# Kernel optimization log

Hardware: AMD Instinct MI355X
Metric: run time of the kernel (lower is better)

## Reference

```python
import jax, jax.numpy as jnp
import numpy as np
import math

H = 16          # num_attention_heads
DH = 64         # attention_head_size
HID = 1024      # hidden_size


def _rotate_half(x):
    # stack([-x[...,1::2], x[...,::2]], -1).reshape_as(x)
    return jnp.stack([-x[..., 1::2], x[..., ::2]], axis=-1).reshape(x.shape)


def _apply_rope(sinusoidal_pos, q, k):
    sin, cos = jnp.split(sinusoidal_pos, 2, axis=-1)            # [1,1,S,DH/2] each
    sin_pos = jnp.stack([sin, sin], axis=-1).reshape(sinusoidal_pos.shape)
    cos_pos = jnp.stack([cos, cos], axis=-1).reshape(sinusoidal_pos.shape)
    q = q * cos_pos + _rotate_half(q) * sin_pos
    k = k * cos_pos + _rotate_half(k) * sin_pos
    return q, k


def _split_heads(x):
    B, S, _ = x.shape
    return x.reshape(B, S, H, DH).transpose(0, 2, 1, 3)         # [B,H,S,DH]


def setup_inputs() -> dict:
    key = jax.random.key(0)
    ks = jax.random.split(key, 5)
    B, S = 4, 2048
    x = jax.random.normal(ks[0], (B, S, HID), dtype=jnp.float32)
    attention_mask = jnp.zeros((B, 1, 1, S), dtype=jnp.float32)
    sinusoidal_pos = jax.random.normal(ks[1], (1, 1, S, DH), dtype=jnp.float32)
    scale = 1.0 / math.sqrt(HID)
    Wq = jax.random.normal(ks[2], (HID, HID), dtype=jnp.float32) * scale
    Wk = jax.random.normal(ks[3], (HID, HID), dtype=jnp.float32) * scale
    Wv = jax.random.normal(ks[4], (HID, HID), dtype=jnp.float32) * scale
    bq = jnp.zeros((HID,), dtype=jnp.float32)
    bk = jnp.zeros((HID,), dtype=jnp.float32)
    bv = jnp.zeros((HID,), dtype=jnp.float32)
    return {"x": x, "attention_mask": attention_mask, "sinusoidal_pos": sinusoidal_pos,
            "Wq": Wq, "bq": bq, "Wk": Wk, "bk": bk, "Wv": Wv, "bv": bv}


def reference(x, attention_mask, sinusoidal_pos, Wq, bq, Wk, bk, Wv, bv):
    # QKV projections (torch Linear: x @ W.T + b)
    q = _split_heads(x @ Wq.T + bq)                             # [B,H,S,DH]
    k = _split_heads(x @ Wk.T + bk)
    v = _split_heads(x @ Wv.T + bv)
    q, k = _apply_rope(sinusoidal_pos, q, k)
    scores = jnp.einsum('bhsd,bhtd->bhst', q, k) / math.sqrt(DH) + attention_mask
    probs = jax.nn.softmax(scores, axis=-1)                     # dropout p=0.0 -> identity
    ctx = jnp.einsum('bhst,bhtd->bhsd', probs, v)               # [B,H,S,DH]
    B, _, S, _ = ctx.shape
    return ctx.transpose(0, 2, 1, 3).reshape(B, S, HID)
```

## Files before the change

kernel.cpp:

```cpp
#include <hip/hip_runtime.h>
#include <stdint.h>

#define BATCH 4
#define SEQ   2048
#define NHEAD 16
#define DHEAD 64
#define HID   1024

typedef __bf16 bf16x8 __attribute__((ext_vector_type(8)));
typedef __bf16 bf16x4 __attribute__((ext_vector_type(4)));
typedef float  f32x4  __attribute__((ext_vector_type(4)));

__device__ __forceinline__ bf16x8 load8f(const float* p) {
  const f32x4 a = ((const f32x4*)p)[0];
  const f32x4 b = ((const f32x4*)p)[1];
  bf16x8 r;
#pragma unroll
  for (int i = 0; i < 4; ++i) r[i] = (__bf16)a[i];
#pragma unroll
  for (int i = 0; i < 4; ++i) r[4 + i] = (__bf16)b[i];
  return r;
}

__device__ __forceinline__ void gload_lds16(const __bf16* g, __bf16* l) {
  __builtin_amdgcn_global_load_lds(
      (const __attribute__((address_space(1))) uint32_t*)g,
      (__attribute__((address_space(3))) uint32_t*)l,
      16, 0, 0);
}

#define XUNITS 1048576
#define WUNITS 131072

__global__ __launch_bounds__(256) void cvt_fused_kernel(
    const float* __restrict__ x,
    const float* __restrict__ Wq, const float* __restrict__ Wk,
    const float* __restrict__ Wv,
    __bf16* __restrict__ xb, __bf16* __restrict__ Wb) {
  const int i = blockIdx.x * 256 + threadIdx.x;
  const float* s;
  __bf16* d;
  if (i < XUNITS) {
    s = x + (size_t)i * 8;
    d = xb + (size_t)i * 8;
  } else {
    const int j = i - XUNITS;
    const int w = j >> 17;
    const int o = j & (WUNITS - 1);
    s = (w == 0 ? Wq : w == 1 ? Wk : Wv) + (size_t)o * 8;
    d = Wb + ((size_t)w << 20) + (size_t)o * 8;
  }
  *(bf16x8*)d = load8f(s);
}

#define ASTRIDE 40
#define BK 32

__global__ __launch_bounds__(512) void qkv_bf16_kernel(
    const __bf16* __restrict__ xb, const __bf16* __restrict__ Wb,
    const float* __restrict__ bq, const float* __restrict__ bk,
    const float* __restrict__ bv, const float* __restrict__ sp,
    float* __restrict__ qout, __bf16* __restrict__ Kws, __bf16* __restrict__ Vws)
{
  const int widx = blockIdx.z;
  const __bf16* __restrict__ W    = Wb + (size_t)widx * HID * HID;
  const float*  __restrict__ bias = (widx == 0) ? bq : (widx == 1) ? bk : bv;

  const int m0   = blockIdx.y * 128;
  const int n0   = blockIdx.x * 128;
  const int tid  = threadIdx.x;
  const int lane = tid & 63;
  const int quad = lane >> 4;
  const int l16  = lane & 15;
  const int wave = tid >> 6;
  const int wr   = wave >> 1, wc = wave & 1;

  __shared__ __align__(16) __bf16 As[2][128 * BK];
  __shared__ __align__(16) __bf16 Bs[2][128 * BK];

  const int srow = wave * 16 + (lane >> 2);
  const int scol = (lane & 3) * 8;
  const __bf16* aglb = xb + (size_t)(m0 + srow) * HID + scol;
  const __bf16* bglb = W  + (size_t)(n0 + srow) * HID + scol;
  const int woff = wave * 512;

  f32x4 acc[2][4];
  const f32x4 z = {0.f, 0.f, 0.f, 0.f};
#pragma unroll
  for (int i = 0; i < 2; ++i)
#pragma unroll
    for (int j = 0; j < 4; ++j) acc[i][j] = z;

  gload_lds16(aglb, &As[0][woff]);
  gload_lds16(bglb, &Bs[0][woff]);
  __syncthreads();

#pragma unroll 1
  for (int k0 = 0; k0 < HID; k0 += 2 * BK) {
    {
      gload_lds16(aglb + (k0 + BK), &As[1][woff]);
      gload_lds16(bglb + (k0 + BK), &Bs[1][woff]);

      bf16x8 af[2], bfr[4];
#pragma unroll
      for (int mt = 0; mt < 2; ++mt)
        af[mt] = *(const bf16x8*)(&As[0][(wr * 32 + mt * 16 + l16) * BK + quad * 8]);
#pragma unroll
      for (int nt = 0; nt < 4; ++nt)
        bfr[nt] = *(const bf16x8*)(&Bs[0][(wc * 64 + nt * 16 + l16) * BK + quad * 8]);

      if (widx < 2) {
#pragma unroll
        for (int mt = 0; mt < 2; ++mt)
#pragma unroll
          for (int nt = 0; nt < 4; ++nt)
            acc[mt][nt] = __builtin_amdgcn_mfma_f32_16x16x32_bf16(af[mt], bfr[nt], acc[mt][nt], 0, 0, 0);
      } else {
#pragma unroll
        for (int mt = 0; mt < 2; ++mt)
#pragma unroll
          for (int nt = 0; nt < 4; ++nt)
            acc[mt][nt] = __builtin_amdgcn_mfma_f32_16x16x32_bf16(bfr[nt], af[mt], acc[mt][nt], 0, 0, 0);
      }
      __syncthreads();
    }
    {
      if (k0 + 2 * BK < HID) {
        gload_lds16(aglb + (k0 + 2 * BK), &As[0][woff]);
        gload_lds16(bglb + (k0 + 2 * BK), &Bs[0][woff]);
      }

      bf16x8 af[2], bfr[4];
#pragma unroll
      for (int mt = 0; mt < 2; ++mt)
        af[mt] = *(const bf16x8*)(&As[1][(wr * 32 + mt * 16 + l16) * BK + quad * 8]);
#pragma unroll
      for (int nt = 0; nt < 4; ++nt)
        bfr[nt] = *(const bf16x8*)(&Bs[1][(wc * 64 + nt * 16 + l16) * BK + quad * 8]);

      if (widx < 2) {
#pragma unroll
        for (int mt = 0; mt < 2; ++mt)
#pragma unroll
          for (int nt = 0; nt < 4; ++nt)
            acc[mt][nt] = __builtin_amdgcn_mfma_f32_16x16x32_bf16(af[mt], bfr[nt], acc[mt][nt], 0, 0, 0);
      } else {
#pragma unroll
        for (int mt = 0; mt < 2; ++mt)
#pragma unroll
          for (int nt = 0; nt < 4; ++nt)
            acc[mt][nt] = __builtin_amdgcn_mfma_f32_16x16x32_bf16(bfr[nt], af[mt], acc[mt][nt], 0, 0, 0);
      }
      __syncthreads();
    }
  }

  if (widx < 2) {
#pragma unroll
    for (int mt = 0; mt < 2; ++mt) {
#pragma unroll
      for (int nt = 0; nt < 4; ++nt) {
        const int n = n0 + wc * 64 + nt * 16 + l16;
        const int h = n >> 6, d = n & 63;
        const float bval = bias[n];
#pragma unroll
        for (int v = 0; v < 4; ++v) {
          const int m = m0 + wr * 32 + mt * 16 + quad * 4 + v;
          const int b = m >> 11, s = m & (SEQ - 1);
          float val = acc[mt][nt][v] + bval;
          float p  = __shfl_xor(val, 1);
          float sn = sp[s * 64 + (d >> 1)];
          float cs = sp[s * 64 + 32 + (d >> 1)];
          val = val * cs + ((d & 1) ? p : -p) * sn;
          if (widx == 0) {
            qout[((size_t)b * SEQ + s) * HID + n] = val;
          } else {
            Kws[(((size_t)b * NHEAD + h) * SEQ + s) * DHEAD + d] = (__bf16)val;
          }
        }
      }
    }
  } else {
#pragma unroll
    for (int mt = 0; mt < 2; ++mt) {
#pragma unroll
      for (int nt = 0; nt < 4; ++nt) {
        const int m = m0 + wr * 32 + mt * 16 + l16;
        const int b = m >> 11, s = m & (SEQ - 1);
#pragma unroll
        for (int v = 0; v < 4; ++v) {
          const int n = n0 + wc * 64 + nt * 16 + quad * 4 + v;
          const int h = n >> 6, d = n & 63;
          float val = acc[mt][nt][v] + bias[n];
          Vws[(((size_t)b * NHEAD + h) * DHEAD + d) * SEQ + s] = (__bf16)val;
        }
      }
    }
  }
}

__global__ __launch_bounds__(512) void qkv_f32_kernel(
    const float* __restrict__ x,
    const float* __restrict__ Wq, const float* __restrict__ bq,
    const float* __restrict__ Wk, const float* __restrict__ bk,
    const float* __restrict__ Wv, const float* __restrict__ bv,
    const float* __restrict__ sp,
    float* __restrict__ qout, __bf16* __restrict__ Kws, __bf16* __restrict__ Vws)
{
  const int widx = blockIdx.z;
  const float* __restrict__ W    = (widx == 0) ? Wq : (widx == 1) ? Wk : Wv;
  const float* __restrict__ bias = (widx == 0) ? bq : (widx == 1) ? bk : bv;

  const int m0   = blockIdx.y * 128;
  const int n0   = blockIdx.x * 128;
  const int tid  = threadIdx.x;
  const int lane = tid & 63;
  const int quad = lane >> 4;
  const int l16  = lane & 15;
  const int wave = tid >> 6;
  const int wr   = wave >> 1, wc = wave & 1;

  __shared__ __align__(16) __bf16 As[128 * ASTRIDE];
  __shared__ __align__(16) __bf16 Bs[128 * ASTRIDE];

  const int srow = tid >> 2;
  const int scb  = tid & 3;

  f32x4 acc[2][4];
  const f32x4 z = {0.f, 0.f, 0.f, 0.f};
#pragma unroll
  for (int i = 0; i < 2; ++i)
#pragma unroll
    for (int j = 0; j < 4; ++j) acc[i][j] = z;

  bf16x8 areg = load8f(x + (size_t)(m0 + srow) * HID + scb * 8);
  bf16x8 breg = load8f(W + (size_t)(n0 + srow) * HID + scb * 8);

  for (int k0 = 0; k0 < HID; k0 += 32) {
    __syncthreads();
    *(bf16x8*)(As + srow * ASTRIDE + scb * 8) = areg;
    *(bf16x8*)(Bs + srow * ASTRIDE + scb * 8) = breg;
    __syncthreads();

    if (k0 + 32 < HID) {
      areg = load8f(x + (size_t)(m0 + srow) * HID + (k0 + 32) + scb * 8);
      breg = load8f(W + (size_t)(n0 + srow) * HID + (k0 + 32) + scb * 8);
    }

    bf16x8 af[2], bfr[4];
#pragma unroll
    for (int mt = 0; mt < 2; ++mt)
      af[mt] = *(const bf16x8*)(As + (wr * 32 + mt * 16 + l16) * ASTRIDE + quad * 8);
#pragma unroll
    for (int nt = 0; nt < 4; ++nt)
      bfr[nt] = *(const bf16x8*)(Bs + (wc * 64 + nt * 16 + l16) * ASTRIDE + quad * 8);

    if (widx < 2) {
#pragma unroll
      for (int mt = 0; mt < 2; ++mt)
#pragma unroll
        for (int nt = 0; nt < 4; ++nt)
          acc[mt][nt] = __builtin_amdgcn_mfma_f32_16x16x32_bf16(af[mt], bfr[nt], acc[mt][nt], 0, 0, 0);
    } else {
#pragma unroll
      for (int mt = 0; mt < 2; ++mt)
#pragma unroll
        for (int nt = 0; nt < 4; ++nt)
          acc[mt][nt] = __builtin_amdgcn_mfma_f32_16x16x32_bf16(bfr[nt], af[mt], acc[mt][nt], 0, 0, 0);
    }
  }

  if (widx < 2) {
#pragma unroll
    for (int mt = 0; mt < 2; ++mt) {
#pragma unroll
      for (int nt = 0; nt < 4; ++nt) {
        const int n = n0 + wc * 64 + nt * 16 + l16;
        const int h = n >> 6, d = n & 63;
        const float bval = bias[n];
#pragma unroll
        for (int v = 0; v < 4; ++v) {
          const int m = m0 + wr * 32 + mt * 16 + quad * 4 + v;
          const int b = m >> 11, s = m & (SEQ - 1);
          float val = acc[mt][nt][v] + bval;
          float p  = __shfl_xor(val, 1);
          float sn = sp[s * 64 + (d >> 1)];
          float cs = sp[s * 64 + 32 + (d >> 1)];
          val = val * cs + ((d & 1) ? p : -p) * sn;
          if (widx == 0) {
            qout[((size_t)b * SEQ + s) * HID + n] = val;
          } else {
            Kws[(((size_t)b * NHEAD + h) * SEQ + s) * DHEAD + d] = (__bf16)val;
          }
        }
      }
    }
  } else {
#pragma unroll
    for (int mt = 0; mt < 2; ++mt) {
#pragma unroll
      for (int nt = 0; nt < 4; ++nt) {
        const int m = m0 + wr * 32 + mt * 16 + l16;
        const int b = m >> 11, s = m & (SEQ - 1);
#pragma unroll
        for (int v = 0; v < 4; ++v) {
          const int n = n0 + wc * 64 + nt * 16 + quad * 4 + v;
          const int h = n >> 6, d = n & 63;
          float val = acc[mt][nt][v] + bias[n];
          Vws[(((size_t)b * NHEAD + h) * DHEAD + d) * SEQ + s] = (__bf16)val;
        }
      }
    }
  }
}

#define KT 64
#define QSTR 72
#define LOG2E 1.44269504088896340736f
#define PSHIFT 12.0f

__global__ __launch_bounds__(512) void attn_kernel(
    float* __restrict__ qo,
    const __bf16* __restrict__ Kws, const __bf16* __restrict__ Vws,
    const float* __restrict__ mask)
{
  const int q0   = blockIdx.x * 128;
  const int bh   = blockIdx.y;
  const int b    = bh >> 4, h = bh & 15;
  const int tid  = threadIdx.x;
  const int lane = tid & 63;
  const int wave = tid >> 6;
  const int quad = lane >> 4;
  const int l16  = lane & 15;

  __shared__ __align__(16) __bf16 Ks[2][64 * QSTR];
  __shared__ __align__(16) __bf16 Vts[2][64 * QSTR];
  __shared__ __align__(16) __bf16 PS[128 * QSTR];

  const __bf16* kbase = Kws + (size_t)bh * SEQ * DHEAD;
  const __bf16* vbase = Vws + (size_t)bh * DHEAD * SEQ;

  bf16x8 qf[2];
#pragma unroll
  for (int ks = 0; ks < 2; ++ks)
    qf[ks] = load8f(qo + ((size_t)b * SEQ + q0 + wave * 16 + l16) * HID
                       + h * DHEAD + ks * 32 + quad * 8);

  f32x4 o_acc[4];
  const f32x4 z = {0.f, 0.f, 0.f, 0.f};
#pragma unroll
  for (int i = 0; i < 4; ++i) o_acc[i] = z;
  float l_part = 0.f;

  const int qrow = tid >> 3;
  const int qcb  = tid & 7;
  const int soff = qrow * QSTR + qcb * 8;

  bf16x8 kreg = *(const bf16x8*)(kbase + (size_t)qrow * DHEAD + qcb * 8);
  bf16x8 vreg = *(const bf16x8*)(vbase + (size_t)qrow * SEQ + qcb * 8);
  *(bf16x8*)(&Ks[0][soff])  = kreg;
  *(bf16x8*)(&Vts[0][soff]) = vreg;
  kreg = *(const bf16x8*)(kbase + (size_t)(KT + qrow) * DHEAD + qcb * 8);
  vreg = *(const bf16x8*)(vbase + (size_t)qrow * SEQ + KT + qcb * 8);
  __syncthreads();

  const float SC2 = 0.125f * LOG2E;
  int cur = 0;

  for (int t0 = 0; t0 < SEQ; t0 += KT) {
    const __bf16* kcur = &Ks[cur][0];
    const __bf16* vcur = &Vts[cur][0];

    if (t0 + KT < SEQ) {
      *(bf16x8*)(&Ks[cur ^ 1][soff])  = kreg;
      *(bf16x8*)(&Vts[cur ^ 1][soff]) = vreg;
    }
    if (t0 + 2 * KT < SEQ) {
      kreg = *(const bf16x8*)(kbase + (size_t)(t0 + 2 * KT + qrow) * DHEAD + qcb * 8);
      vreg = *(const bf16x8*)(vbase + (size_t)qrow * SEQ + (t0 + 2 * KT) + qcb * 8);
    }

    f32x4 sc[4];
#pragma unroll
    for (int nt = 0; nt < 4; ++nt) sc[nt] = z;

    __builtin_amdgcn_s_setprio(1);
#pragma unroll
    for (int ks = 0; ks < 2; ++ks) {
      bf16x8 kf[4];
#pragma unroll
      for (int nt = 0; nt < 4; ++nt)
        kf[nt] = *(const bf16x8*)(kcur + (nt * 16 + l16) * QSTR + ks * 32 + quad * 8);
#pragma unroll
      for (int nt = 0; nt < 4; ++nt)
        sc[nt] = __builtin_amdgcn_mfma_f32_16x16x32_bf16(kf[nt], qf[ks], sc[nt], 0, 0, 0);
    }
    __builtin_amdgcn_s_setprio(0);

    f32x4 mv4[4];
#pragma unroll
    for (int nt = 0; nt < 4; ++nt)
      mv4[nt] = *(const f32x4*)(mask + b * SEQ + t0 + nt * 16 + quad * 4);

    const int prow = wave * 16 + l16;
#pragma unroll
    for (int nt = 0; nt < 4; ++nt) {
      bf16x4 pk;
#pragma unroll
      for (int v = 0; v < 4; ++v) {
        const float p = __builtin_amdgcn_exp2f(sc[nt][v] * SC2 + mv4[nt][v] * LOG2E - PSHIFT);
        l_part += p;
        pk[v] = (__bf16)p;
      }
      *(bf16x4*)(PS + prow * QSTR + nt * 16 + quad * 4) = pk;
    }

    __builtin_amdgcn_s_setprio(1);
#pragma unroll
    for (int ks2 = 0; ks2 < 2; ++ks2) {
      bf16x8 pf = *(const bf16x8*)(PS + prow * QSTR + ks2 * 32 + quad * 8);
      bf16x8 vf[4];
#pragma unroll
      for (int db = 0; db < 4; ++db)
        vf[db] = *(const bf16x8*)(vcur + (db * 16 + l16) * QSTR + ks2 * 32 + quad * 8);
#pragma unroll
      for (int db = 0; db < 4; ++db)
        o_acc[db] = __builtin_amdgcn_mfma_f32_16x16x32_bf16(vf[db], pf, o_acc[db], 0, 0, 0);
    }
    __builtin_amdgcn_s_setprio(0);

    __syncthreads();
    cur ^= 1;
  }

  l_part += __shfl_xor(l_part, 16);
  l_part += __shfl_xor(l_part, 32);
  const float inv = 1.0f / l_part;

  const int s = q0 + wave * 16 + l16;
  float* op = qo + ((size_t)b * SEQ + s) * HID + h * DHEAD + quad * 4;
#pragma unroll
  for (int db = 0; db < 4; ++db) {
    f32x4 val = o_acc[db];
    val[0] *= inv; val[1] *= inv; val[2] *= inv; val[3] *= inv;
    *(f32x4*)(op + db * 16) = val;
  }
}

extern "C" void kernel_launch(void* const* d_in, const int* in_sizes, int n_in,
                              void* d_out, int out_size, void* d_ws, size_t ws_size,
                              hipStream_t stream) {
  const float* x    = (const float*)d_in[0];
  const float* mask = (const float*)d_in[1];
  const float* sp   = (const float*)d_in[2];
  const float* Wq   = (const float*)d_in[3];
  const float* bq   = (const float*)d_in[4];
  const float* Wk   = (const float*)d_in[5];
  const float* bk   = (const float*)d_in[6];
  const float* Wv   = (const float*)d_in[7];
  const float* bv   = (const float*)d_in[8];
  float* out = (float*)d_out;

  const size_t per = (size_t)BATCH * NHEAD * SEQ * DHEAD;
  const size_t wel = (size_t)3 * HID * HID;
  __bf16* Kws = (__bf16*)d_ws;
  __bf16* Vws = Kws + per;

  const size_t need = (2 * per + per + wel) * sizeof(__bf16);
  if (ws_size >= need) {
    __bf16* xb = Vws + per;
    __bf16* Wb = xb + per;
    cvt_fused_kernel<<<5632, 256, 0, stream>>>(x, Wq, Wk, Wv, xb, Wb);
    qkv_bf16_kernel<<<dim3(8, 64, 3), 512, 0, stream>>>(
        xb, Wb, bq, bk, bv, sp, out, Kws, Vws);
  } else {
    qkv_f32_kernel<<<dim3(8, 64, 3), 512, 0, stream>>>(
        x, Wq, bq, Wk, bk, Wv, bv, sp, out, Kws, Vws);
  }
  attn_kernel<<<dim3(16, 64), 512, 0, stream>>>(out, Kws, Vws, mask);
}
```

Baseline: 308.0 us.

## Load K/V fragments directly from global into registers, drop LDS staging

The attention kernel stops staging K and V tiles through double-buffered shared memory and instead has each wave load its MFMA fragments straight from global memory into registers. One register array is reused for K and then V, and the next K tile is loaded at the end of each iteration. The block shrinks to 256 threads covering 64 queries, and the grid doubles, so the per-tile __syncthreads goes away and LDS use drops. In exchange, each wave now reads K/V itself, with no sharing across waves in a block, so global/L2 traffic rises. Load latency is only partly hidden by issuing loads ahead of their use.

After: 662.8 us. 2.15x slower.

```diff
diff --git a/kernel.cpp b/kernel.cpp
--- a/kernel.cpp
+++ b/kernel.cpp
@@ -319,12 +319,12 @@
 #define LOG2E 1.44269504088896340736f
 #define PSHIFT 12.0f
 
-__global__ __launch_bounds__(512) void attn_kernel(
+__global__ __launch_bounds__(256) void attn_kernel(
     float* __restrict__ qo,
     const __bf16* __restrict__ Kws, const __bf16* __restrict__ Vws,
     const float* __restrict__ mask)
 {
-  const int q0   = blockIdx.x * 128;
+  const int q0   = blockIdx.x * 64;
   const int bh   = blockIdx.y;
   const int b    = bh >> 4, h = bh & 15;
   const int tid  = threadIdx.x;
@@ -333,9 +333,7 @@
   const int quad = lane >> 4;
   const int l16  = lane & 15;
 
-  __shared__ __align__(16) __bf16 Ks[2][64 * QSTR];
-  __shared__ __align__(16) __bf16 Vts[2][64 * QSTR];
-  __shared__ __align__(16) __bf16 PS[128 * QSTR];
+  __shared__ __align__(16) __bf16 PS[64 * QSTR];
 
   const __bf16* kbase = Kws + (size_t)bh * SEQ * DHEAD;
   const __bf16* vbase = Vws + (size_t)bh * DHEAD * SEQ;
@@ -352,57 +350,45 @@
   for (int i = 0; i < 4; ++i) o_acc[i] = z;
   float l_part = 0.f;
 
-  const int qrow = tid >> 3;
-  const int qcb  = tid & 7;
-  const int soff = qrow * QSTR + qcb * 8;
-
-  bf16x8 kreg = *(const bf16x8*)(kbase + (size_t)qrow * DHEAD + qcb * 8);
-  bf16x8 vreg = *(const bf16x8*)(vbase + (size_t)qrow * SEQ + qcb * 8);
-  *(bf16x8*)(&Ks[0][soff])  = kreg;
-  *(bf16x8*)(&Vts[0][soff]) = vreg;
-  kreg = *(const bf16x8*)(kbase + (size_t)(KT + qrow) * DHEAD + qcb * 8);
-  vreg = *(const bf16x8*)(vbase + (size_t)qrow * SEQ + KT + qcb * 8);
-  __syncthreads();
+  const __bf16* kfb = kbase + (size_t)l16 * DHEAD + quad * 8;
+  const __bf16* vfb = vbase + (size_t)l16 * SEQ + quad * 8;
+
+  bf16x8 kv[2][4];
+
+#pragma unroll
+  for (int ks = 0; ks < 2; ++ks)
+#pragma unroll
+    for (int nt = 0; nt < 4; ++nt)
+      kv[ks][nt] = *(const bf16x8*)(kfb + (size_t)(nt * 16) * DHEAD + ks * 32);
 
   const float SC2 = 0.125f * LOG2E;
-  int cur = 0;
-
+  const int prow = wave * 16 + l16;
+
+#pragma unroll 1
   for (int t0 = 0; t0 < SEQ; t0 += KT) {
-    const __bf16* kcur = &Ks[cur][0];
-    const __bf16* vcur = &Vts[cur][0];
-
-    if (t0 + KT < SEQ) {
-      *(bf16x8*)(&Ks[cur ^ 1][soff])  = kreg;
-      *(bf16x8*)(&Vts[cur ^ 1][soff]) = vreg;
-    }
-    if (t0 + 2 * KT < SEQ) {
-      kreg = *(const bf16x8*)(kbase + (size_t)(t0 + 2 * KT + qrow) * DHEAD + qcb * 8);
-      vreg = *(const bf16x8*)(vbase + (size_t)qrow * SEQ + (t0 + 2 * KT) + qcb * 8);
-    }
-
     f32x4 sc[4];
 #pragma unroll
     for (int nt = 0; nt < 4; ++nt) sc[nt] = z;
 
     __builtin_amdgcn_s_setprio(1);
 #pragma unroll
-    for (int ks = 0; ks < 2; ++ks) {
-      bf16x8 kf[4];
+    for (int ks = 0; ks < 2; ++ks)
 #pragma unroll
       for (int nt = 0; nt < 4; ++nt)
-        kf[nt] = *(const bf16x8*)(kcur + (nt * 16 + l16) * QSTR + ks * 32 + quad * 8);
-#pragma unroll
-      for (int nt = 0; nt < 4; ++nt)
-        sc[nt] = __builtin_amdgcn_mfma_f32_16x16x32_bf16(kf[nt], qf[ks], sc[nt], 0, 0, 0);
-    }
+        sc[nt] = __builtin_amdgcn_mfma_f32_16x16x32_bf16(kv[ks][nt], qf[ks], sc[nt], 0, 0, 0);
     __builtin_amdgcn_s_setprio(0);
+
+#pragma unroll
+    for (int ks2 = 0; ks2 < 2; ++ks2)
+#pragma unroll
+      for (int db = 0; db < 4; ++db)
+        kv[ks2][db] = *(const bf16x8*)(vfb + (size_t)(db * 16) * SEQ + t0 + ks2 * 32);
 
     f32x4 mv4[4];
 #pragma unroll
     for (int nt = 0; nt < 4; ++nt)
       mv4[nt] = *(const f32x4*)(mask + b * SEQ + t0 + nt * 16 + quad * 4);
 
-    const int prow = wave * 16 + l16;
 #pragma unroll
     for (int nt = 0; nt < 4; ++nt) {
       bf16x4 pk;
@@ -419,18 +405,19 @@
 #pragma unroll
     for (int ks2 = 0; ks2 < 2; ++ks2) {
       bf16x8 pf = *(const bf16x8*)(PS + prow * QSTR + ks2 * 32 + quad * 8);
-      bf16x8 vf[4];
 #pragma unroll
       for (int db = 0; db < 4; ++db)
-        vf[db] = *(const bf16x8*)(vcur + (db * 16 + l16) * QSTR + ks2 * 32 + quad * 8);
-#pragma unroll
-      for (int db = 0; db < 4; ++db)
-        o_acc[db] = __builtin_amdgcn_mfma_f32_16x16x32_bf16(vf[db], pf, o_acc[db], 0, 0, 0);
+        o_acc[db] = __builtin_amdgcn_mfma_f32_16x16x32_bf16(kv[ks2][db], pf, o_acc[db], 0, 0, 0);
     }
     __builtin_amdgcn_s_setprio(0);
 
-    __syncthreads();
-    cur ^= 1;
+    if (t0 + KT < SEQ) {
+#pragma unroll
+      for (int ks = 0; ks < 2; ++ks)
+#pragma unroll
+        for (int nt = 0; nt < 4; ++nt)
+          kv[ks][nt] = *(const bf16x8*)(kfb + (size_t)(t0 + KT + nt * 16) * DHEAD + ks * 32);
+    }
   }
 
   l_part += __shfl_xor(l_part, 16);
@@ -477,5 +464,5 @@
     qkv_f32_kernel<<<dim3(8, 64, 3), 512, 0, stream>>>(
         x, Wq, bq, Wk, bk, Wv, bv, sp, out, Kws, Vws);
   }
-  attn_kernel<<<dim3(16, 64), 512, 0, stream>>>(out, Kws, Vws, mask);
-}
+  attn_kernel<<<dim3(32, 64), 256, 0, stream>>>(out, Kws, Vws, mask);
+}
```

## Enlarge QKV GEMM M-tile to 256 and single-buffer attention K/V tiles

Applied to the files above, without the earlier changes.

The bf16 QKV projection kernel now computes a 256x128 output tile per block, with each wave holding 4x4 MFMA accumulators, and the grid is halved in M. This raises arithmetic intensity per LDS load and reuses each loaded W tile across twice as many rows, at the cost of more registers (launch bounds hint of 4). Separately, the attention kernel drops double-buffered K/V LDS tiles for a single buffer with a register prefetch, cutting LDS use but adding a barrier between the store and the compute.

Result: slower. 742.5 us (+141.1%).

```diff
diff --git a/kernel.cpp b/kernel.cpp
--- a/kernel.cpp
+++ b/kernel.cpp
@@ -56,7 +56,7 @@
 #define ASTRIDE 40
 #define BK 32
 
-__global__ __launch_bounds__(512) void qkv_bf16_kernel(
+__global__ __launch_bounds__(512, 4) void qkv_bf16_kernel(
     const __bf16* __restrict__ xb, const __bf16* __restrict__ Wb,
     const float* __restrict__ bq, const float* __restrict__ bk,
     const float* __restrict__ bv, const float* __restrict__ sp,
@@ -66,6 +66,159 @@
   const __bf16* __restrict__ W    = Wb + (size_t)widx * HID * HID;
   const float*  __restrict__ bias = (widx == 0) ? bq : (widx == 1) ? bk : bv;
 
+  const int m0   = blockIdx.y * 256;
+  const int n0   = blockIdx.x * 128;
+  const int tid  = threadIdx.x;
+  const int lane = tid & 63;
+  const int quad = lane >> 4;
+  const int l16  = lane & 15;
+  const int wave = tid >> 6;
+  const int wr   = wave >> 1, wc = wave & 1;
+
+  __shared__ __align__(16) __bf16 As[2][256 * BK];
+  __shared__ __align__(16) __bf16 Bs[2][128 * BK];
+
+  const int arow0 = wave * 32 + (lane >> 2);
+  const int arow1 = wave * 32 + 16 + (lane >> 2);
+  const int brow  = wave * 16 + (lane >> 2);
+  const int scol  = (lane & 3) * 8;
+  const __bf16* aglb0 = xb + (size_t)(m0 + arow0) * HID + scol;
+  const __bf16* aglb1 = xb + (size_t)(m0 + arow1) * HID + scol;
+  const __bf16* bglb  = W  + (size_t)(n0 + brow) * HID + scol;
+  const int aoff0 = wave * 1024;
+  const int aoff1 = wave * 1024 + 512;
+  const int boff  = wave * 512;
+
+  f32x4 acc[4][4];
+  const f32x4 z = {0.f, 0.f, 0.f, 0.f};
+#pragma unroll
+  for (int i = 0; i < 4; ++i)
+#pragma unroll
+    for (int j = 0; j < 4; ++j) acc[i][j] = z;
+
+  gload_lds16(aglb0, &As[0][aoff0]);
+  gload_lds16(aglb1, &As[0][aoff1]);
+  gload_lds16(bglb,  &Bs[0][boff]);
+  __syncthreads();
+
+#pragma unroll 1
+  for (int k0 = 0; k0 < HID; k0 += 2 * BK) {
+    {
+      gload_lds16(aglb0 + (k0 + BK), &As[1][aoff0]);
+      gload_lds16(aglb1 + (k0 + BK), &As[1][aoff1]);
+      gload_lds16(bglb  + (k0 + BK), &Bs[1][boff]);
+
+      bf16x8 af[4], bfr[4];
+#pragma unroll
+      for (int mt = 0; mt < 4; ++mt)
+        af[mt] = *(const bf16x8*)(&As[0][(wr * 64 + mt * 16 + l16) * BK + quad * 8]);
+#pragma unroll
+      for (int nt = 0; nt < 4; ++nt)
+        bfr[nt] = *(const bf16x8*)(&Bs[0][(wc * 64 + nt * 16 + l16) * BK + quad * 8]);
+
+      if (widx < 2) {
+#pragma unroll
+        for (int mt = 0; mt < 4; ++mt)
+#pragma unroll
+          for (int nt = 0; nt < 4; ++nt)
+            acc[mt][nt] = __builtin_amdgcn_mfma_f32_16x16x32_bf16(af[mt], bfr[nt], acc[mt][nt], 0, 0, 0);
+      } else {
+#pragma unroll
+        for (int mt = 0; mt < 4; ++mt)
+#pragma unroll
+          for (int nt = 0; nt < 4; ++nt)
+            acc[mt][nt] = __builtin_amdgcn_mfma_f32_16x16x32_bf16(bfr[nt], af[mt], acc[mt][nt], 0, 0, 0);
+      }
+      __syncthreads();
+    }
+    {
+      if (k0 + 2 * BK < HID) {
+        gload_lds16(aglb0 + (k0 + 2 * BK), &As[0][aoff0]);
+        gload_lds16(aglb1 + (k0 + 2 * BK), &As[0][aoff1]);
+        gload_lds16(bglb  + (k0 + 2 * BK), &Bs[0][boff]);
+      }
+
+      bf16x8 af[4], bfr[4];
+#pragma unroll
+      for (int mt = 0; mt < 4; ++mt)
+        af[mt] = *(const bf16x8*)(&As[1][(wr * 64 + mt * 16 + l16) * BK + quad * 8]);
+#pragma unroll
+      for (int nt = 0; nt < 4; ++nt)
+        bfr[nt] = *(const bf16x8*)(&Bs[1][(wc * 64 + nt * 16 + l16) * BK + quad * 8]);
+
+      if (widx < 2) {
+#pragma unroll
+        for (int mt = 0; mt < 4; ++mt)
+#pragma unroll
+          for (int nt = 0; nt < 4; ++nt)
+            acc[mt][nt] = __builtin_amdgcn_mfma_f32_16x16x32_bf16(af[mt], bfr[nt], acc[mt][nt], 0, 0, 0);
+      } else {
+#pragma unroll
+        for (int mt = 0; mt < 4; ++mt)
+#pragma unroll
+          for (int nt = 0; nt < 4; ++nt)
+            acc[mt][nt] = __builtin_amdgcn_mfma_f32_16x16x32_bf16(bfr[nt], af[mt], acc[mt][nt], 0, 0, 0);
+      }
+      __syncthreads();
+    }
+  }
+
+  if (widx < 2) {
+#pragma unroll
+    for (int mt = 0; mt < 4; ++mt) {
+#pragma unroll
+      for (int nt = 0; nt < 4; ++nt) {
+        const int n = n0 + wc * 64 + nt * 16 + l16;
+        const int h = n >> 6, d = n & 63;
+        const float bval = bias[n];
+#pragma unroll
+        for (int v = 0; v < 4; ++v) {
+          const int m = m0 + wr * 64 + mt * 16 + quad * 4 + v;
+          const int b = m >> 11, s = m & (SEQ - 1);
+          float val = acc[mt][nt][v] + bval;
+          float p  = __shfl_xor(val, 1);
+          float sn = sp[s * 64 + (d >> 1)];
+          float cs = sp[s * 64 + 32 + (d >> 1)];
+          val = val * cs + ((d & 1) ? p : -p) * sn;
+          if (widx == 0) {
+            qout[((size_t)b * SEQ + s) * HID + n] = val;
+          } else {
+            Kws[(((size_t)b * NHEAD + h) * SEQ + s) * DHEAD + d] = (__bf16)val;
+          }
+        }
+      }
+    }
+  } else {
+#pragma unroll
+    for (int mt = 0; mt < 4; ++mt) {
+#pragma unroll
+      for (int nt = 0; nt < 4; ++nt) {
+        const int m = m0 + wr * 64 + mt * 16 + l16;
+        const int b = m >> 11, s = m & (SEQ - 1);
+#pragma unroll
+        for (int v = 0; v < 4; ++v) {
+          const int n = n0 + wc * 64 + nt * 16 + quad * 4 + v;
+          const int h = n >> 6, d = n & 63;
+          float val = acc[mt][nt][v] + bias[n];
+          Vws[(((size_t)b * NHEAD + h) * DHEAD + d) * SEQ + s] = (__bf16)val;
+        }
+      }
+    }
+  }
+}
+
+__global__ __launch_bounds__(512) void qkv_f32_kernel(
+    const float* __restrict__ x,
+    const float* __restrict__ Wq, const float* __restrict__ bq,
+    const float* __restrict__ Wk, const float* __restrict__ bk,
+    const float* __restrict__ Wv, const float* __restrict__ bv,
+    const float* __restrict__ sp,
+    float* __restrict__ qout, __bf16* __restrict__ Kws, __bf16* __restrict__ Vws)
+{
+  const int widx = blockIdx.z;
+  const float* __restrict__ W    = (widx == 0) ? Wq : (widx == 1) ? Wk : Wv;
+  const float* __restrict__ bias = (widx == 0) ? bq : (widx == 1) ? bk : bv;
+
   const int m0   = blockIdx.y * 128;
   const int n0   = blockIdx.x * 128;
   const int tid  = threadIdx.x;
@@ -75,14 +228,11 @@
   const int wave = tid >> 6;
   const int wr   = wave >> 1, wc = wave & 1;
 
-  __shared__ __align__(16) __bf16 As[2][128 * BK];
-  __shared__ __align__(16) __bf16 Bs[2][128 * BK];
-
-  const int srow = wave * 16 + (lane >> 2);
-  const int scol = (lane & 3) * 8;
-  const __bf16* aglb = xb + (size_t)(m0 + srow) * HID + scol;
-  const __bf16* bglb = W  + (size_t)(n0 + srow) * HID + scol;
-  const int woff = wave * 512;
+  __shared__ __align__(16) __bf16 As[128 * ASTRIDE];
+  __shared__ __align__(16) __bf16 Bs[128 * ASTRIDE];
+
+  const int srow = tid >> 2;
+  const int scb  = tid & 3;
 
   f32x4 acc[2][4];
   const f32x4 z = {0.f, 0.f, 0.f, 0.f};
@@ -91,67 +241,40 @@
 #pragma unroll
     for (int j = 0; j < 4; ++j) acc[i][j] = z;
 
-  gload_lds16(aglb, &As[0][woff]);
-  gload_lds16(bglb, &Bs[0][woff]);
-  __syncthreads();
-
-#pragma unroll 1
-  for (int k0 = 0; k0 < HID; k0 += 2 * BK) {
-    {
-      gload_lds16(aglb + (k0 + BK), &As[1][woff]);
-      gload_lds16(bglb + (k0 + BK), &Bs[1][woff]);
-
-      bf16x8 af[2], bfr[4];
+  bf16x8 areg = load8f(x + (size_t)(m0 + srow) * HID + scb * 8);
+  bf16x8 breg = load8f(W + (size_t)(n0 + srow) * HID + scb * 8);
+
+  for (int k0 = 0; k0 < HID; k0 += 32) {
+    __syncthreads();
+    *(bf16x8*)(As + srow * ASTRIDE + scb * 8) = areg;
+    *(bf16x8*)(Bs + srow * ASTRIDE + scb * 8) = breg;
+    __syncthreads();
+
+    if (k0 + 32 < HID) {
+      areg = load8f(x + (size_t)(m0 + srow) * HID + (k0 + 32) + scb * 8);
+      breg = load8f(W + (size_t)(n0 + srow) * HID + (k0 + 32) + scb * 8);
+    }
+
+    bf16x8 af[2], bfr[4];
+#pragma unroll
+    for (int mt = 0; mt < 2; ++mt)
+      af[mt] = *(const bf16x8*)(As + (wr * 32 + mt * 16 + l16) * ASTRIDE + quad * 8);
+#pragma unroll
+    for (int nt = 0; nt < 4; ++nt)
+      bfr[nt] = *(const bf16x8*)(Bs + (wc * 64 + nt * 16 + l16) * ASTRIDE + quad * 8);
+
+    if (widx < 2) {
 #pragma unroll
       for (int mt = 0; mt < 2; ++mt)
-        af[mt] = *(const bf16x8*)(&As[0][(wr * 32 + mt * 16 + l16) * BK + quad * 8]);
-#pragma unroll
-      for (int nt = 0; nt < 4; ++nt)
-        bfr[nt] = *(const bf16x8*)(&Bs[0][(wc * 64 + nt * 16 + l16) * BK + quad * 8]);
-
-      if (widx < 2) {
-#pragma unroll
-        for (int mt = 0; mt < 2; ++mt)
-#pragma unroll
-          for (int nt = 0; nt < 4; ++nt)
-            acc[mt][nt] = __builtin_amdgcn_mfma_f32_16x16x32_bf16(af[mt], bfr[nt], acc[mt][nt], 0, 0, 0);
-      } else {
-#pragma unroll
-        for (int mt = 0; mt < 2; ++mt)
-#pragma unroll
-          for (int nt = 0; nt < 4; ++nt)
-            acc[mt][nt] = __builtin_amdgcn_mfma_f32_16x16x32_bf16(bfr[nt], af[mt], acc[mt][nt], 0, 0, 0);
-      }
-      __syncthreads();
-    }
-    {
-      if (k0 + 2 * BK < HID) {
-        gload_lds16(aglb + (k0 + 2 * BK), &As[0][woff]);
-        gload_lds16(bglb + (k0 + 2 * BK), &Bs[0][woff]);
-      }
-
-      bf16x8 af[2], bfr[4];
+#pragma unroll
+        for (int nt = 0; nt < 4; ++nt)
+          acc[mt][nt] = __builtin_amdgcn_mfma_f32_16x16x32_bf16(af[mt], bfr[nt], acc[mt][nt], 0, 0, 0);
+    } else {
 #pragma unroll
       for (int mt = 0; mt < 2; ++mt)
-        af[mt] = *(const bf16x8*)(&As[1][(wr * 32 + mt * 16 + l16) * BK + quad * 8]);
-#pragma unroll
-      for (int nt = 0; nt < 4; ++nt)
-        bfr[nt] = *(const bf16x8*)(&Bs[1][(wc * 64 + nt * 16 + l16) * BK + quad * 8]);
-
-      if (widx < 2) {
-#pragma unroll
-        for (int mt = 0; mt < 2; ++mt)
-#pragma unroll
-          for (int nt = 0; nt < 4; ++nt)
-            acc[mt][nt] = __builtin_amdgcn_mfma_f32_16x16x32_bf16(af[mt], bfr[nt], acc[mt][nt], 0, 0, 0);
-      } else {
-#pragma unroll
-        for (int mt = 0; mt < 2; ++mt)
-#pragma unroll
-          for (int nt = 0; nt < 4; ++nt)
-            acc[mt][nt] = __builtin_amdgcn_mfma_f32_16x16x32_bf16(bfr[nt], af[mt], acc[mt][nt], 0, 0, 0);
-      }
-      __syncthreads();
+#pragma unroll
+        for (int nt = 0; nt < 4; ++nt)
+          acc[mt][nt] = __builtin_amdgcn_mfma_f32_16x16x32_bf16(bfr[nt], af[mt], acc[mt][nt], 0, 0, 0);
     }
   }
 
@@ -199,121 +322,6 @@
   }
 }
 
-__global__ __launch_bounds__(512) void qkv_f32_kernel(
-    const float* __restrict__ x,
-    const float* __restrict__ Wq, const float* __restrict__ bq,
-    const float* __restrict__ Wk, const float* __restrict__ bk,
-    const float* __restrict__ Wv, const float* __restrict__ bv,
-    const float* __restrict__ sp,
-    float* __restrict__ qout, __bf16* __restrict__ Kws, __bf16* __restrict__ Vws)
-{
-  const int widx = blockIdx.z;
-  const float* __restrict__ W    = (widx == 0) ? Wq : (widx == 1) ? Wk : Wv;
-  const float* __restrict__ bias = (widx == 0) ? bq : (widx == 1) ? bk : bv;
-
-  const int m0   = blockIdx.y * 128;
-  const int n0   = blockIdx.x * 128;
-  const int tid  = threadIdx.x;
-  const int lane = tid & 63;
-  const int quad = lane >> 4;
-  const int l16  = lane & 15;
-  const int wave = tid >> 6;
-  const int wr   = wave >> 1, wc = wave & 1;
-
-  __shared__ __align__(16) __bf16 As[128 * ASTRIDE];
-  __shared__ __align__(16) __bf16 Bs[128 * ASTRIDE];
-
-  const int srow = tid >> 2;
-  const int scb  = tid & 3;
-
-  f32x4 acc[2][4];
-  const f32x4 z = {0.f, 0.f, 0.f, 0.f};
-#pragma unroll
-  for (int i = 0; i < 2; ++i)
-#pragma unroll
-    for (int j = 0; j < 4; ++j) acc[i][j] = z;
-
-  bf16x8 areg = load8f(x + (size_t)(m0 + srow) * HID + scb * 8);
-  bf16x8 breg = load8f(W + (size_t)(n0 + srow) * HID + scb * 8);
-
-  for (int k0 = 0; k0 < HID; k0 += 32) {
-    __syncthreads();
-    *(bf16x8*)(As + srow * ASTRIDE + scb * 8) = areg;
-    *(bf16x8*)(Bs + srow * ASTRIDE + scb * 8) = breg;
-    __syncthreads();
-
-    if (k0 + 32 < HID) {
-      areg = load8f(x + (size_t)(m0 + srow) * HID + (k0 + 32) + scb * 8);
-      breg = load8f(W + (size_t)(n0 + srow) * HID + (k0 + 32) + scb * 8);
-    }
-
-    bf16x8 af[2], bfr[4];
-#pragma unroll
-    for (int mt = 0; mt < 2; ++mt)
-      af[mt] = *(const bf16x8*)(As + (wr * 32 + mt * 16 + l16) * ASTRIDE + quad * 8);
-#pragma unroll
-    for (int nt = 0; nt < 4; ++nt)
-      bfr[nt] = *(const bf16x8*)(Bs + (wc * 64 + nt * 16 + l16) * ASTRIDE + quad * 8);
-
-    if (widx < 2) {
-#pragma unroll
-      for (int mt = 0; mt < 2; ++mt)
-#pragma unroll
-        for (int nt = 0; nt < 4; ++nt)
-          acc[mt][nt] = __builtin_amdgcn_mfma_f32_16x16x32_bf16(af[mt], bfr[nt], acc[mt][nt], 0, 0, 0);
-    } else {
-#pragma unroll
-      for (int mt = 0; mt < 2; ++mt)
-#pragma unroll
-        for (int nt = 0; nt < 4; ++nt)
-          acc[mt][nt] = __builtin_amdgcn_mfma_f32_16x16x32_bf16(bfr[nt], af[mt], acc[mt][nt], 0, 0, 0);
-    }
-  }
-
-  if (widx < 2) {
-#pragma unroll
-    for (int mt = 0; mt < 2; ++mt) {
-#pragma unroll
-      for (int nt = 0; nt < 4; ++nt) {
-        const int n = n0 + wc * 64 + nt * 16 + l16;
-        const int h = n >> 6, d = n & 63;
-        const float bval = bias[n];
-#pragma unroll
-        for (int v = 0; v < 4; ++v) {
-          const int m = m0 + wr * 32 + mt * 16 + quad * 4 + v;
-          const int b = m >> 11, s = m & (SEQ - 1);
-          float val = acc[mt][nt][v] + bval;
-          float p  = __shfl_xor(val, 1);
-          float sn = sp[s * 64 + (d >> 1)];
-          float cs = sp[s * 64 + 32 + (d >> 1)];
-          val = val * cs + ((d & 1) ? p : -p) * sn;
-          if (widx == 0) {
-            qout[((size_t)b * SEQ + s) * HID + n] = val;
-          } else {
-            Kws[(((size_t)b * NHEAD + h) * SEQ + s) * DHEAD + d] = (__bf16)val;
-          }
-        }
-      }
-    }
-  } else {
-#pragma unroll
-    for (int mt = 0; mt < 2; ++mt) {
-#pragma unroll
-      for (int nt = 0; nt < 4; ++nt) {
-        const int m = m0 + wr * 32 + mt * 16 + l16;
-        const int b = m >> 11, s = m & (SEQ - 1);
-#pragma unroll
-        for (int v = 0; v < 4; ++v) {
-          const int n = n0 + wc * 64 + nt * 16 + quad * 4 + v;
-          const int h = n >> 6, d = n & 63;
-          float val = acc[mt][nt][v] + bias[n];
-          Vws[(((size_t)b * NHEAD + h) * DHEAD + d) * SEQ + s] = (__bf16)val;
-        }
-      }
-    }
-  }
-}
-
 #define KT 64
 #define QSTR 72
 #define LOG2E 1.44269504088896340736f
@@ -333,8 +341,8 @@
   const int quad = lane >> 4;
   const int l16  = lane & 15;
 
-  __shared__ __align__(16) __bf16 Ks[2][64 * QSTR];
-  __shared__ __align__(16) __bf16 Vts[2][64 * QSTR];
+  __shared__ __align__(16) __bf16 Ks[64 * QSTR];
+  __shared__ __align__(16) __bf16 Vts[64 * QSTR];
   __shared__ __align__(16) __bf16 PS[128 * QSTR];
 
   const __bf16* kbase = Kws + (size_t)bh * SEQ * DHEAD;
@@ -354,30 +362,20 @@
 
   const int qrow = tid >> 3;
   const int qcb  = tid & 7;
-  const int soff = qrow * QSTR + qcb * 8;
 
   bf16x8 kreg = *(const bf16x8*)(kbase + (size_t)qrow * DHEAD + qcb * 8);
   bf16x8 vreg = *(const bf16x8*)(vbase + (size_t)qrow * SEQ + qcb * 8);
-  *(bf16x8*)(&Ks[0][soff])  = kreg;
-  *(bf16x8*)(&Vts[0][soff]) = vreg;
-  kreg = *(const bf16x8*)(kbase + (size_t)(KT + qrow) * DHEAD + qcb * 8);
-  vreg = *(const bf16x8*)(vbase + (size_t)qrow * SEQ + KT + qcb * 8);
-  __syncthreads();
 
   const float SC2 = 0.125f * LOG2E;
-  int cur = 0;
 
   for (int t0 = 0; t0 < SEQ; t0 += KT) {
-    const __bf16* kcur = &Ks[cur][0];
-    const __bf16* vcur = &Vts[cur][0];
+    *(bf16x8*)(Ks  + qrow * QSTR + qcb * 8) = kreg;
+    *(bf16x8*)(Vts + qrow * QSTR + qcb * 8) = vreg;
+    __syncthreads();
 
     if (t0 + KT < SEQ) {
-      *(bf16x8*)(&Ks[cur ^ 1][soff])  = kreg;
-      *(bf16x8*)(&Vts[cur ^ 1][soff]) = vreg;
-    }
-    if (t0 + 2 * KT < SEQ) {
-      kreg = *(const bf16x8*)(kbase + (size_t)(t0 + 2 * KT + qrow) * DHEAD + qcb * 8);
-      vreg = *(const bf16x8*)(vbase + (size_t)qrow * SEQ + (t0 + 2 * KT) + qcb * 8);
+      kreg = *(const bf16x8*)(kbase + (size_t)(t0 + KT + qrow) * DHEAD + qcb * 8);
+      vreg = *(const bf16x8*)(vbase + (size_t)qrow * SEQ + (t0 + KT) + qcb * 8);
     }
 
     f32x4 sc[4];
@@ -390,7 +388,7 @@
       bf16x8 kf[4];
 #pragma unroll
       for (int nt = 0; nt < 4; ++nt)
-        kf[nt] = *(const bf16x8*)(kcur + (nt * 16 + l16) * QSTR + ks * 32 + quad * 8);
+        kf[nt] = *(const bf16x8*)(Ks + (nt * 16 + l16) * QSTR + ks * 32 + quad * 8);
 #pragma unroll
       for (int nt = 0; nt < 4; ++nt)
         sc[nt] = __builtin_amdgcn_mfma_f32_16x16x32_bf16(kf[nt], qf[ks], sc[nt], 0, 0, 0);
@@ -422,15 +420,13 @@
       bf16x8 vf[4];
 #pragma unroll
       for (int db = 0; db < 4; ++db)
-        vf[db] = *(const bf16x8*)(vcur + (db * 16 + l16) * QSTR + ks2 * 32 + quad * 8);
+        vf[db] = *(const bf16x8*)(Vts + (db * 16 + l16) * QSTR + ks2 * 32 + quad * 8);
 #pragma unroll
       for (int db = 0; db < 4; ++db)
         o_acc[db] = __builtin_amdgcn_mfma_f32_16x16x32_bf16(vf[db], pf, o_acc[db], 0, 0, 0);
     }
     __builtin_amdgcn_s_setprio(0);
-
     __syncthreads();
-    cur ^= 1;
   }
 
   l_part += __shfl_xor(l_part, 16);
@@ -471,7 +467,7 @@
     __bf16* xb = Vws + per;
     __bf16* Wb = xb + per;
     cvt_fused_kernel<<<5632, 256, 0, stream>>>(x, Wq, Wk, Wv, xb, Wb);
-    qkv_bf16_kernel<<<dim3(8, 64, 3), 512, 0, stream>>>(
+    qkv_bf16_kernel<<<dim3(8, 32, 3), 512, 0, stream>>>(
         xb, Wb, bq, bk, bv, sp, out, Kws, Vws);
   } else {
     qkv_f32_kernel<<<dim3(8, 64, 3), 512, 0, stream>>>(
```

## Swizzle block order for XCD locality and single-buffer attention K/V tiles

Applied to the files above, without the earlier changes.

Remaps block indices in the QKV GEMM and attention kernels so that blocks sharing the same weights or the same (batch, head) K/V land on the same XCD, improving L2 reuse across the chiplets. The attention kernel also drops double-buffered K/V shared memory in favour of a single buffer with an extra barrier per tile, which reduces LDS use and may raise occupancy. The cost is less overlap between global loads and compute, plus an added synchronisation per iteration. A local variable is renamed to avoid shadowing the new swizzle index.

Result: faster. 299.4 us (-2.8%).

```diff
diff --git a/kernel.cpp b/kernel.cpp
--- a/kernel.cpp
+++ b/kernel.cpp
@@ -66,8 +66,11 @@
   const __bf16* __restrict__ W    = Wb + (size_t)widx * HID * HID;
   const float*  __restrict__ bias = (widx == 0) ? bq : (widx == 1) ? bk : bv;
 
-  const int m0   = blockIdx.y * 128;
-  const int n0   = blockIdx.x * 128;
+  const int d    = blockIdx.x + (blockIdx.y << 3);
+  const int t    = (d & 7) * 64 + (d >> 3);
+  const int n0   = (t & 7) * 128;
+  const int m0   = (t >> 3) * 128;
+
   const int tid  = threadIdx.x;
   const int lane = tid & 63;
   const int quad = lane >> 4;
@@ -161,7 +164,7 @@
 #pragma unroll
       for (int nt = 0; nt < 4; ++nt) {
         const int n = n0 + wc * 64 + nt * 16 + l16;
-        const int h = n >> 6, d = n & 63;
+        const int h = n >> 6, dd = n & 63;
         const float bval = bias[n];
 #pragma unroll
         for (int v = 0; v < 4; ++v) {
@@ -169,13 +172,13 @@
           const int b = m >> 11, s = m & (SEQ - 1);
           float val = acc[mt][nt][v] + bval;
           float p  = __shfl_xor(val, 1);
-          float sn = sp[s * 64 + (d >> 1)];
-          float cs = sp[s * 64 + 32 + (d >> 1)];
-          val = val * cs + ((d & 1) ? p : -p) * sn;
+          float sn = sp[s * 64 + (dd >> 1)];
+          float cs = sp[s * 64 + 32 + (dd >> 1)];
+          val = val * cs + ((dd & 1) ? p : -p) * sn;
           if (widx == 0) {
             qout[((size_t)b * SEQ + s) * HID + n] = val;
           } else {
-            Kws[(((size_t)b * NHEAD + h) * SEQ + s) * DHEAD + d] = (__bf16)val;
+            Kws[(((size_t)b * NHEAD + h) * SEQ + s) * DHEAD + dd] = (__bf16)val;
           }
         }
       }
@@ -190,9 +193,9 @@
 #pragma unroll
         for (int v = 0; v < 4; ++v) {
           const int n = n0 + wc * 64 + nt * 16 + quad * 4 + v;
-          const int h = n >> 6, d = n & 63;
+          const int h = n >> 6, dd = n & 63;
           float val = acc[mt][nt][v] + bias[n];
-          Vws[(((size_t)b * NHEAD + h) * DHEAD + d) * SEQ + s] = (__bf16)val;
+          Vws[(((size_t)b * NHEAD + h) * DHEAD + dd) * SEQ + s] = (__bf16)val;
         }
       }
     }
@@ -276,7 +279,7 @@
 #pragma unroll
       for (int nt = 0; nt < 4; ++nt) {
         const int n = n0 + wc * 64 + nt * 16 + l16;
-        const int h = n >> 6, d = n & 63;
+        const int h = n >> 6, dd = n & 63;
         const float bval = bias[n];
 #pragma unroll
         for (int v = 0; v < 4; ++v) {
@@ -284,13 +287,13 @@
           const int b = m >> 11, s = m & (SEQ - 1);
           float val = acc[mt][nt][v] + bval;
           float p  = __shfl_xor(val, 1);
-          float sn = sp[s * 64 + (d >> 1)];
-          float cs = sp[s * 64 + 32 + (d >> 1)];
-          val = val * cs + ((d & 1) ? p : -p) * sn;
+          float sn = sp[s * 64 + (dd >> 1)];
+          float cs = sp[s * 64 + 32 + (dd >> 1)];
+          val = val * cs + ((dd & 1) ? p : -p) * sn;
           if (widx == 0) {
             qout[((size_t)b * SEQ + s) * HID + n] = val;
           } else {
-            Kws[(((size_t)b * NHEAD + h) * SEQ + s) * DHEAD + d] = (__bf16)val;
+            Kws[(((size_t)b * NHEAD + h) * SEQ + s) * DHEAD + dd] = (__bf16)val;
           }
         }
       }
@@ -305,9 +308,9 @@
 #pragma unroll
         for (int v = 0; v < 4; ++v) {
           const int n = n0 + wc * 64 + nt * 16 + quad * 4 + v;
-          const int h = n >> 6, d = n & 63;
+          const int h = n >> 6, dd = n & 63;
           float val = acc[mt][nt][v] + bias[n];
-          Vws[(((size_t)b * NHEAD + h) * DHEAD + d) * SEQ + s] = (__bf16)val;
+          Vws[(((size_t)b * NHEAD + h) * DHEAD + dd) * SEQ + s] = (__bf16)val;
         }
       }
     }
@@ -324,8 +327,11 @@
     const __bf16* __restrict__ Kws, const __bf16* __restrict__ Vws,
     const float* __restrict__ mask)
 {
-  const int q0   = blockIdx.x * 128;
-  const int bh   = blockIdx.y;
+  const int dsw  = blockIdx.x + (blockIdx.y << 4);
+  const int tsw  = (dsw & 7) * 128 + (dsw >> 3);
+  const int bh   = tsw >> 4;
+  const int q0   = (tsw & 15) * 128;
+
   const int b    = bh >> 4, h = bh & 15;
   const int tid  = threadIdx.x;
   const int lane = tid & 63;
@@ -333,8 +339,8 @@
   const int quad = lane >> 4;
   const int l16  = lane & 15;
 
-  __shared__ __align__(16) __bf16 Ks[2][64 * QSTR];
-  __shared__ __align__(16) __bf16 Vts[2][64 * QSTR];
+  __shared__ __align__(16) __bf16 Ks[64 * QSTR];
+  __shared__ __align__(16) __bf16 Vts[64 * QSTR];
   __shared__ __align__(16) __bf16 PS[128 * QSTR];
 
   const __bf16* kbase = Kws + (size_t)bh * SEQ * DHEAD;
@@ -354,30 +360,20 @@
 
   const int qrow = tid >> 3;
   const int qcb  = tid & 7;
-  const int soff = qrow * QSTR + qcb * 8;
 
   bf16x8 kreg = *(const bf16x8*)(kbase + (size_t)qrow * DHEAD + qcb * 8);
   bf16x8 vreg = *(const bf16x8*)(vbase + (size_t)qrow * SEQ + qcb * 8);
-  *(bf16x8*)(&Ks[0][soff])  = kreg;
-  *(bf16x8*)(&Vts[0][soff]) = vreg;
-  kreg = *(const bf16x8*)(kbase + (size_t)(KT + qrow) * DHEAD + qcb * 8);
-  vreg = *(const bf16x8*)(vbase + (size_t)qrow * SEQ + KT + qcb * 8);
-  __syncthreads();
 
   const float SC2 = 0.125f * LOG2E;
-  int cur = 0;
 
   for (int t0 = 0; t0 < SEQ; t0 += KT) {
-    const __bf16* kcur = &Ks[cur][0];
-    const __bf16* vcur = &Vts[cur][0];
+    *(bf16x8*)(Ks  + qrow * QSTR + qcb * 8) = kreg;
+    *(bf16x8*)(Vts + qrow * QSTR + qcb * 8) = vreg;
+    __syncthreads();
 
     if (t0 + KT < SEQ) {
-      *(bf16x8*)(&Ks[cur ^ 1][soff])  = kreg;
-      *(bf16x8*)(&Vts[cur ^ 1][soff]) = vreg;
-    }
-    if (t0 + 2 * KT < SEQ) {
-      kreg = *(const bf16x8*)(kbase + (size_t)(t0 + 2 * KT + qrow) * DHEAD + qcb * 8);
-      vreg = *(const bf16x8*)(vbase + (size_t)qrow * SEQ + (t0 + 2 * KT) + qcb * 8);
+      kreg = *(const bf16x8*)(kbase + (size_t)(t0 + KT + qrow) * DHEAD + qcb * 8);
+      vreg = *(const bf16x8*)(vbase + (size_t)qrow * SEQ + (t0 + KT) + qcb * 8);
     }
 
     f32x4 sc[4];
@@ -390,7 +386,7 @@
       bf16x8 kf[4];
 #pragma unroll
       for (int nt = 0; nt < 4; ++nt)
-        kf[nt] = *(const bf16x8*)(kcur + (nt * 16 + l16) * QSTR + ks * 32 + quad * 8);
+        kf[nt] = *(const bf16x8*)(Ks + (nt * 16 + l16) * QSTR + ks * 32 + quad * 8);
 #pragma unroll
       for (int nt = 0; nt < 4; ++nt)
         sc[nt] = __builtin_amdgcn_mfma_f32_16x16x32_bf16(kf[nt], qf[ks], sc[nt], 0, 0, 0);
@@ -422,15 +418,13 @@
       bf16x8 vf[4];
 #pragma unroll
       for (int db = 0; db < 4; ++db)
-        vf[db] = *(const bf16x8*)(vcur + (db * 16 + l16) * QSTR + ks2 * 32 + quad * 8);
+        vf[db] = *(const bf16x8*)(Vts + (db * 16 + l16) * QSTR + ks2 * 32 + quad * 8);
 #pragma unroll
       for (int db = 0; db < 4; ++db)
         o_acc[db] = __builtin_amdgcn_mfma_f32_16x16x32_bf16(vf[db], pf, o_acc[db], 0, 0, 0);
     }
     __builtin_amdgcn_s_setprio(0);
-
     __syncthreads();
-    cur ^= 1;
   }
 
   l_part += __shfl_xor(l_part, 16);
```
